# Kernel tuning notes

Hardware: AMD Instinct MI355X
Metric: run time of the kernel (lower is better)

## Reference

```python
import jax, jax.numpy as jnp
import numpy as np

D_MODEL = 1024
N_HEADS = 16
D_K = D_MODEL // N_HEADS  # 64
D_V = D_MODEL // N_HEADS  # 64
B, S = 2, 2048


def setup_inputs() -> dict:
    key = jax.random.key(0)
    ks = jax.random.split(key, 8)
    inp = {
        "Q": jax.random.normal(ks[0], (B, S, D_MODEL), dtype=jnp.float32),
        "K": jax.random.normal(ks[1], (B, S, D_MODEL), dtype=jnp.float32),
        "V": jax.random.normal(ks[2], (B, S, D_MODEL), dtype=jnp.float32),
        "prev": jax.random.normal(ks[3], (B, N_HEADS, S, S), dtype=jnp.float32) * 0.1,
        # torch nn.Linear weights are [out_features, in_features]
        "W_Q": jax.random.normal(ks[4], (N_HEADS * D_K, D_MODEL), dtype=jnp.float32) / np.sqrt(D_MODEL),
        "W_K": jax.random.normal(ks[5], (N_HEADS * D_K, D_MODEL), dtype=jnp.float32) / np.sqrt(D_MODEL),
        "W_V": jax.random.normal(ks[6], (N_HEADS * D_V, D_MODEL), dtype=jnp.float32) / np.sqrt(D_MODEL),
        "W_O": jax.random.normal(ks[7], (D_MODEL, N_HEADS * D_V), dtype=jnp.float32) / np.sqrt(N_HEADS * D_V),
    }
    return inp


def reference(Q, K, V, prev, W_Q, W_K, W_V, W_O):
    scale = D_K ** (-0.5)
    # projections: x @ W.T, then split heads -> (b, h, s, d)
    q = jnp.einsum('bsm,em->bse', Q, W_Q).reshape(B, S, N_HEADS, D_K).transpose(0, 2, 1, 3)
    k = jnp.einsum('bsm,em->bse', K, W_K).reshape(B, S, N_HEADS, D_K).transpose(0, 2, 1, 3)
    v = jnp.einsum('bsm,em->bse', V, W_V).reshape(B, S, N_HEADS, D_V).transpose(0, 2, 1, 3)
    scores = jnp.einsum('bhqd,bhkd->bhqk', q, k) * scale + prev
    attn = jax.nn.softmax(scores, axis=-1)  # attn_dropout = 0 (eval)
    context = jnp.einsum('bhqk,bhkd->bhqd', attn, v)
    context = context.transpose(0, 2, 1, 3).reshape(B, S, N_HEADS * D_V)
    output = jnp.einsum('bse,me->bsm', context, W_O)  # proj_dropout = 0 (eval)
    return (output, attn, scores)
```

## Files before the change

kernel.cpp:

```cpp
#include <hip/hip_runtime.h>

#define S_LEN 2048
#define NH 16
#define DH 64
#define DM 1024
#define NB 2
#define BS 4096

typedef __attribute__((ext_vector_type(4))) float f32x4;
typedef __attribute__((ext_vector_type(8))) short bfrag;

__device__ __forceinline__ unsigned short f2bf(float f) {
    unsigned u = __builtin_bit_cast(unsigned, f);
    u += 0x7FFFu + ((u >> 16) & 1u);
    return (unsigned short)(u >> 16);
}

__device__ __forceinline__ void gld16(const unsigned short* g, unsigned short* l) {
    __builtin_amdgcn_global_load_lds((const __attribute__((address_space(1))) void*)g,
                                     (__attribute__((address_space(3))) void*)l, 16, 0, 0);
}

__device__ __forceinline__ void lds_fence() {
    asm volatile("s_waitcnt lgkmcnt(0)" ::: "memory");
    __builtin_amdgcn_sched_barrier(0);
}

__global__ __launch_bounds__(256) void cast_all(const float* __restrict__ Q,
                                                const float* __restrict__ K,
                                                const float* __restrict__ V,
                                                const float* __restrict__ Wq,
                                                const float* __restrict__ Wk,
                                                const float* __restrict__ Wv,
                                                const float* __restrict__ Wo,
                                                unsigned short* __restrict__ Qc,
                                                unsigned short* __restrict__ Kc,
                                                unsigned short* __restrict__ Vc,
                                                unsigned short* __restrict__ Wqc,
                                                unsigned short* __restrict__ Wkc,
                                                unsigned short* __restrict__ Wvc,
                                                unsigned short* __restrict__ Woc) {
    int i = blockIdx.x * 256 + threadIdx.x;
    const float* src;
    unsigned short* dst;
    int off;
    if (i < 3145728) {
        int w = i >> 20;
        off = i & 1048575;
        src = (w == 0) ? Q : (w == 1) ? K : V;
        dst = (w == 0) ? Qc : (w == 1) ? Kc : Vc;
    } else {
        int j = i - 3145728;
        int w = j >> 18;
        off = j & 262143;
        src = (w == 0) ? Wq : (w == 1) ? Wk : (w == 2) ? Wv : Wo;
        dst = (w == 0) ? Wqc : (w == 1) ? Wkc : (w == 2) ? Wvc : Woc;
    }
    float4 v = reinterpret_cast<const float4*>(src)[off];
    ushort4 o;
    o.x = f2bf(v.x); o.y = f2bf(v.y); o.z = f2bf(v.z); o.w = f2bf(v.w);
    reinterpret_cast<ushort4*>(dst)[off] = o;
}

__global__ __launch_bounds__(256) void gemm_qkv(const unsigned short* __restrict__ Qc,
                                                const unsigned short* __restrict__ Kc,
                                                const unsigned short* __restrict__ Vc,
                                                const unsigned short* __restrict__ Wqc,
                                                const unsigned short* __restrict__ Wkc,
                                                const unsigned short* __restrict__ Wvc,
                                                unsigned short* __restrict__ qh,
                                                unsigned short* __restrict__ kh,
                                                unsigned short* __restrict__ vT) {
    const int z = blockIdx.z;
    const unsigned short* A = (z == 0) ? Qc : (z == 1) ? Kc : Vc;
    const unsigned short* B = (z == 0) ? Wqc : (z == 1) ? Wkc : Wvc;
    const int tid = threadIdx.x, lane = tid & 63;
    const int l15 = lane & 15, lhi = lane >> 4;
    const int w = tid >> 6, wr = w >> 1, wc = w & 1;
    const int m0 = blockIdx.y * 128, n0 = blockIdx.x * 128;
    const int K = DM;
    const int lr8 = lane >> 3;
    const int csw = (lane & 7) ^ lr8;

    __shared__ unsigned short sA[128 * 64];
    __shared__ unsigned short sB[128 * 64];

    f32x4 acc[4][4];
#pragma unroll
    for (int i = 0; i < 4; ++i)
#pragma unroll
        for (int j = 0; j < 4; ++j) acc[i][j] = (f32x4){0.f, 0.f, 0.f, 0.f};

    for (int t = 0; t < 16; ++t) {
        const int k0 = t * 64;
#pragma unroll
        for (int i = 0; i < 4; ++i) {
            int g = w * 4 + i;
            int row = g * 8 + lr8;
            gld16(A + (size_t)(m0 + row) * K + k0 + csw * 8, sA + g * 512);
            gld16(B + (size_t)(n0 + row) * K + k0 + csw * 8, sB + g * 512);
        }
        __syncthreads();
#pragma unroll
        for (int kk = 0; kk < 2; ++kk) {
            bfrag a[4], b[4];
#pragma unroll
            for (int f = 0; f < 4; ++f) {
                int ra = wr * 64 + f * 16 + l15;
                a[f] = *reinterpret_cast<const bfrag*>(
                    sA + ra * 64 + (((kk * 4 + lhi) ^ (ra & 7)) << 3));
                int rb = wc * 64 + f * 16 + l15;
                b[f] = *reinterpret_cast<const bfrag*>(
                    sB + rb * 64 + (((kk * 4 + lhi) ^ (rb & 7)) << 3));
            }
#pragma unroll
            for (int fm = 0; fm < 4; ++fm)
#pragma unroll
                for (int fn = 0; fn < 4; ++fn)
                    acc[fm][fn] =
                        __builtin_amdgcn_mfma_f32_16x16x32_bf16(a[fm], b[fn], acc[fm][fn], 0, 0, 0);
        }
        __syncthreads();
    }

    if (z == 2) {
#pragma unroll
        for (int fm = 0; fm < 4; ++fm)
#pragma unroll
            for (int fn = 0; fn < 4; ++fn) {
                int sbase = m0 + wr * 64 + fm * 16 + (lhi << 2);
                int gcol = n0 + wc * 64 + fn * 16 + l15;
                int b = sbase >> 11, s = sbase & 2047, h = gcol >> 6, d = gcol & 63;
                ushort4 o;
                o.x = f2bf(acc[fm][fn][0]); o.y = f2bf(acc[fm][fn][1]);
                o.z = f2bf(acc[fm][fn][2]); o.w = f2bf(acc[fm][fn][3]);
                *reinterpret_cast<ushort4*>(vT + ((size_t)(b * NH + h) * DH + d) * S_LEN + s) = o;
            }
    } else {
        unsigned short* Out = (z == 0) ? qh : kh;
#pragma unroll
        for (int fm = 0; fm < 4; ++fm)
#pragma unroll
            for (int fn = 0; fn < 4; ++fn)
#pragma unroll
                for (int r = 0; r < 4; ++r) {
                    int grow = m0 + wr * 64 + fm * 16 + (lhi << 2) + r;
                    int gcol = n0 + wc * 64 + fn * 16 + l15;
                    int b = grow >> 11, s = grow & 2047, h = gcol >> 6, d = gcol & 63;
                    Out[((size_t)(b * NH + h) * S_LEN + s) * DH + d] = f2bf(acc[fm][fn][r]);
                }
    }
}

__global__ __launch_bounds__(256) void gemm_out(const unsigned short* __restrict__ A,
                                                const unsigned short* __restrict__ B,
                                                float* __restrict__ Out) {
    const int tid = threadIdx.x, lane = tid & 63;
    const int l15 = lane & 15, lhi = lane >> 4;
    const int w = tid >> 6, wr = w >> 1, wc = w & 1;
    const int m0 = blockIdx.y * 128, n0 = blockIdx.x * 128;
    const int K = DM, N = DM;
    const int lr8 = lane >> 3;
    const int csw = (lane & 7) ^ lr8;

    __shared__ unsigned short sA[128 * 64];
    __shared__ unsigned short sB[128 * 64];

    f32x4 acc[4][4];
#pragma unroll
    for (int i = 0; i < 4; ++i)
#pragma unroll
        for (int j = 0; j < 4; ++j) acc[i][j] = (f32x4){0.f, 0.f, 0.f, 0.f};

    for (int t = 0; t < 16; ++t) {
        const int k0 = t * 64;
#pragma unroll
        for (int i = 0; i < 4; ++i) {
            int g = w * 4 + i;
            int row = g * 8 + lr8;
            gld16(A + (size_t)(m0 + row) * K + k0 + csw * 8, sA + g * 512);
            gld16(B + (size_t)(n0 + row) * K + k0 + csw * 8, sB + g * 512);
        }
        __syncthreads();
#pragma unroll
        for (int kk = 0; kk < 2; ++kk) {
            bfrag a[4], b[4];
#pragma unroll
            for (int f = 0; f < 4; ++f) {
                int ra = wr * 64 + f * 16 + l15;
                a[f] = *reinterpret_cast<const bfrag*>(
                    sA + ra * 64 + (((kk * 4 + lhi) ^ (ra & 7)) << 3));
                int rb = wc * 64 + f * 16 + l15;
                b[f] = *reinterpret_cast<const bfrag*>(
                    sB + rb * 64 + (((kk * 4 + lhi) ^ (rb & 7)) << 3));
            }
#pragma unroll
            for (int fm = 0; fm < 4; ++fm)
#pragma unroll
                for (int fn = 0; fn < 4; ++fn)
                    acc[fm][fn] =
                        __builtin_amdgcn_mfma_f32_16x16x32_bf16(a[fm], b[fn], acc[fm][fn], 0, 0, 0);
        }
        __syncthreads();
    }

#pragma unroll
    for (int fm = 0; fm < 4; ++fm)
#pragma unroll
        for (int fn = 0; fn < 4; ++fn)
#pragma unroll
            for (int r = 0; r < 4; ++r) {
                int grow = m0 + wr * 64 + fm * 16 + (lhi << 2) + r;
                int gcol = n0 + wc * 64 + fn * 16 + l15;
                Out[(size_t)grow * N + gcol] = acc[fm][fn][r];
            }
}

__global__ __launch_bounds__(64, 3) void attn_fused(const unsigned short* __restrict__ qh,
                                                    const unsigned short* __restrict__ kh,
                                                    const unsigned short* __restrict__ vT,
                                                    const float* __restrict__ prev,
                                                    float* __restrict__ scores,
                                                    float* __restrict__ attn,
                                                    unsigned short* __restrict__ ctx) {
    const int z = blockIdx.z;
    const int m0 = blockIdx.x * 16;
    const int lane = threadIdx.x & 63;
    const int l15 = lane & 15, lhi = lane >> 4;
    const int crow = lane >> 4;
    const int ccol = (lane & 15) * 4;

    __shared__ float sT[16 * 64];
    unsigned short* sB = reinterpret_cast<unsigned short*>(sT);

    const unsigned short* Qz = qh + (size_t)z * S_LEN * DH;
    const unsigned short* Kz = kh + (size_t)z * S_LEN * DH;
    const unsigned short* Vz = vT + (size_t)z * DH * S_LEN;
    const size_t zbase = (size_t)z * S_LEN * S_LEN;
    const float scale = 0.125f;

    size_t ro[4];
#pragma unroll
    for (int i = 0; i < 4; ++i)
        ro[i] = zbase + (size_t)(m0 + i * 4 + crow) * S_LEN + ccol;

    bfrag qf[2];
#pragma unroll
    for (int kk = 0; kk < 2; ++kk)
        qf[kk] = *reinterpret_cast<const bfrag*>(Qz + (size_t)(m0 + l15) * DH + kk * 32 +
                                                 lhi * 8);

    float m_r[4], l_r[4];
#pragma unroll
    for (int i = 0; i < 4; ++i) { m_r[i] = -1e30f; l_r[i] = 0.f; }

    bfrag kf[2][4];
#pragma unroll
    for (int kk = 0; kk < 2; ++kk)
#pragma unroll
        for (int f = 0; f < 4; ++f)
            kf[kk][f] = *reinterpret_cast<const bfrag*>(
                Kz + (size_t)(f * 16 + l15) * DH + kk * 32 + lhi * 8);
    f32x4 pv4[4];
#pragma unroll
    for (int i = 0; i < 4; ++i)
        pv4[i] = __builtin_nontemporal_load(reinterpret_cast<const f32x4*>(prev + ro[i]));

    for (int kt = 0; kt < 32; ++kt) {
        const int n0 = kt * 64;

        f32x4 acc[4];
#pragma unroll
        for (int f = 0; f < 4; ++f) acc[f] = (f32x4){0.f, 0.f, 0.f, 0.f};
#pragma unroll
        for (int kk = 0; kk < 2; ++kk)
#pragma unroll
            for (int f = 0; f < 4; ++f)
                acc[f] = __builtin_amdgcn_mfma_f32_16x16x32_bf16(kf[kk][f], qf[kk], acc[f], 0, 0, 0);

        if (kt < 31) {
            const int n1 = n0 + 64;
#pragma unroll
            for (int kk = 0; kk < 2; ++kk)
#pragma unroll
                for (int f = 0; f < 4; ++f)
                    kf[kk][f] = *reinterpret_cast<const bfrag*>(
                        Kz + (size_t)(n1 + f * 16 + l15) * DH + kk * 32 + lhi * 8);
        }

#pragma unroll
        for (int f = 0; f < 4; ++f)
            *reinterpret_cast<f32x4*>(sT + l15 * 64 + (((f * 4 + lhi) ^ (l15 & 7)) * 4)) = acc[f];
        lds_fence();
        f32x4 sc[4];
#pragma unroll
        for (int i = 0; i < 4; ++i) {
            int r = i * 4 + crow;
            sc[i] = *reinterpret_cast<const f32x4*>(sT + r * 64 + ((l15 ^ (r & 7)) * 4));
        }

#pragma unroll
        for (int i = 0; i < 4; ++i)
#pragma unroll
            for (int r = 0; r < 4; ++r) sc[i][r] = sc[i][r] * scale + pv4[i][r];
        if (kt < 31) {
            const int n1 = n0 + 64;
#pragma unroll
            for (int i = 0; i < 4; ++i)
                pv4[i] = __builtin_nontemporal_load(
                    reinterpret_cast<const f32x4*>(prev + ro[i] + n1));
        }
#pragma unroll
        for (int i = 0; i < 4; ++i)
            *reinterpret_cast<f32x4*>(scores + ro[i] + n0) = sc[i];

#pragma unroll
        for (int i = 0; i < 4; ++i) {
            float pm = fmaxf(fmaxf(sc[i][0], sc[i][1]), fmaxf(sc[i][2], sc[i][3]));
            pm = fmaxf(pm, __shfl_xor(pm, 1));
            pm = fmaxf(pm, __shfl_xor(pm, 2));
            pm = fmaxf(pm, __shfl_xor(pm, 4));
            pm = fmaxf(pm, __shfl_xor(pm, 8));
            float mnew = fmaxf(m_r[i], pm);
            float ps = __expf(sc[i][0] - mnew) + __expf(sc[i][1] - mnew) +
                       __expf(sc[i][2] - mnew) + __expf(sc[i][3] - mnew);
            ps += __shfl_xor(ps, 1);
            ps += __shfl_xor(ps, 2);
            ps += __shfl_xor(ps, 4);
            ps += __shfl_xor(ps, 8);
            l_r[i] = l_r[i] * __expf(m_r[i] - mnew) + ps;
            m_r[i] = mnew;
        }
    }

    float inv_l[4];
#pragma unroll
    for (int i = 0; i < 4; ++i) inv_l[i] = 1.0f / l_r[i];

    f32x4 acco[4];
#pragma unroll
    for (int f = 0; f < 4; ++f) acco[f] = (f32x4){0.f, 0.f, 0.f, 0.f};

    bfrag vf[2][4];
#pragma unroll
    for (int kk = 0; kk < 2; ++kk)
#pragma unroll
        for (int f = 0; f < 4; ++f)
            vf[kk][f] = *reinterpret_cast<const bfrag*>(
                Vz + (size_t)(f * 16 + l15) * S_LEN + 31 * 64 + kk * 32 + lhi * 8);
    f32x4 sv[4];
#pragma unroll
    for (int i = 0; i < 4; ++i)
        sv[i] = *reinterpret_cast<const f32x4*>(scores + ro[i] + 31 * 64);

    for (int kt = 31; kt >= 0; --kt) {
        const int n0 = kt * 64;
#pragma unroll
        for (int i = 0; i < 4; ++i) {
            int r = i * 4 + crow;
            f32x4 p4;
#pragma unroll
            for (int rr = 0; rr < 4; ++rr) p4[rr] = __expf(sv[i][rr] - m_r[i]) * inv_l[i];
            __builtin_nontemporal_store(p4, reinterpret_cast<f32x4*>(attn + ro[i] + n0));
            ushort4 pb;
            pb.x = f2bf(p4[0]); pb.y = f2bf(p4[1]); pb.z = f2bf(p4[2]); pb.w = f2bf(p4[3]);
            *reinterpret_cast<ushort4*>(sB + r * 64 + ((l15 ^ (r & 7)) * 4)) = pb;
        }
        lds_fence();
        bfrag pf[2];
#pragma unroll
        for (int kk = 0; kk < 2; ++kk) {
            int c0 = kk * 8 + lhi * 2;
            ushort4 lo = *reinterpret_cast<const ushort4*>(sB + l15 * 64 + ((c0 ^ (l15 & 7)) * 4));
            ushort4 hi =
                *reinterpret_cast<const ushort4*>(sB + l15 * 64 + (((c0 + 1) ^ (l15 & 7)) * 4));
            pf[kk][0] = (short)lo.x; pf[kk][1] = (short)lo.y;
            pf[kk][2] = (short)lo.z; pf[kk][3] = (short)lo.w;
            pf[kk][4] = (short)hi.x; pf[kk][5] = (short)hi.y;
            pf[kk][6] = (short)hi.z; pf[kk][7] = (short)hi.w;
        }
        if (kt > 0) {
            const int n1 = n0 - 64;
#pragma unroll
            for (int i = 0; i < 4; ++i)
                sv[i] = *reinterpret_cast<const f32x4*>(scores + ro[i] + n1);
        }
#pragma unroll
        for (int kk = 0; kk < 2; ++kk)
#pragma unroll
            for (int f = 0; f < 4; ++f)
                acco[f] = __builtin_amdgcn_mfma_f32_16x16x32_bf16(vf[kk][f], pf[kk], acco[f], 0, 0, 0);
        if (kt > 0) {
            const int n1 = n0 - 64;
#pragma unroll
            for (int kk = 0; kk < 2; ++kk)
#pragma unroll
                for (int f = 0; f < 4; ++f)
                    vf[kk][f] = *reinterpret_cast<const bfrag*>(
                        Vz + (size_t)(f * 16 + l15) * S_LEN + n1 + kk * 32 + lhi * 8);
        }
    }

    const int b = z >> 4, h = z & 15;
    const int s = m0 + l15;
#pragma unroll
    for (int f = 0; f < 4; ++f) {
        int d0 = f * 16 + lhi * 4;
        ushort4 o;
        o.x = f2bf(acco[f][0]); o.y = f2bf(acco[f][1]);
        o.z = f2bf(acco[f][2]); o.w = f2bf(acco[f][3]);
        *reinterpret_cast<ushort4*>(ctx + ((size_t)(b * S_LEN + s)) * DM + h * DH + d0) = o;
    }
}

extern "C" void kernel_launch(void* const* d_in, const int* in_sizes, int n_in, void* d_out,
                              int out_size, void* d_ws, size_t ws_size, hipStream_t stream) {
    const float* Q = (const float*)d_in[0];
    const float* K = (const float*)d_in[1];
    const float* V = (const float*)d_in[2];
    const float* prev = (const float*)d_in[3];
    const float* Wq = (const float*)d_in[4];
    const float* Wk = (const float*)d_in[5];
    const float* Wv = (const float*)d_in[6];
    const float* Wo = (const float*)d_in[7];

    float* out = (float*)d_out;
    float* attn = out + (size_t)BS * DM;
    float* scores = attn + (size_t)NB * NH * S_LEN * S_LEN;

    unsigned short* ws = (unsigned short*)d_ws;
    unsigned short* Qc = ws;
    unsigned short* Kc = Qc + (size_t)BS * DM;
    unsigned short* Vc = Kc + (size_t)BS * DM;
    unsigned short* Wqc = Vc + (size_t)BS * DM;
    unsigned short* Wkc = Wqc + (size_t)DM * DM;
    unsigned short* Wvc = Wkc + (size_t)DM * DM;
    unsigned short* Woc = Wvc + (size_t)DM * DM;
    unsigned short* qh = Woc + (size_t)DM * DM;
    unsigned short* kh = qh + (size_t)BS * DM;
    unsigned short* vT = kh + (size_t)BS * DM;
    unsigned short* ctx = vT + (size_t)BS * DM;

    cast_all<<<16384, 256, 0, stream>>>(Q, K, V, Wq, Wk, Wv, Wo,
                                        Qc, Kc, Vc, Wqc, Wkc, Wvc, Woc);

    dim3 gq(DM / 128, BS / 128, 3);
    gemm_qkv<<<gq, 256, 0, stream>>>(Qc, Kc, Vc, Wqc, Wkc, Wvc, qh, kh, vT);

    dim3 ga(S_LEN / 16, 1, NB * NH);
    attn_fused<<<ga, 64, 0, stream>>>(qh, kh, vT, prev, scores, attn, ctx);

    dim3 gp(DM / 128, BS / 128, 1);
    gemm_out<<<gp, 256, 0, stream>>>(ctx, Woc, out);
}
```

Measured before the change: 631.4 us.

## Split fused attention into scores/stats and softmax-PV kernels with 4-wave blocks

Splits the single-wave fused attention kernel into two kernels. The first computes scores and stores the per-row max and sum to a workspace buffer; the second recomputes the probabilities, writes attn and does the PV matmul. Blocks grow to 4 waves, and the second kernel is launched in reverse block order, likely so it reads recently written scores while they may still be in cache. Software prefetching of the K, V, prev and scores tiles is dropped in favour of plain in-loop loads. This adds a kernel launch and a small stats round trip.

Result: slower. 646.8 us (+2.4%).

```diff
diff --git a/kernel.cpp b/kernel.cpp
--- a/kernel.cpp
+++ b/kernel.cpp
@@ -216,26 +216,25 @@
             }
 }
 
-__global__ __launch_bounds__(64, 3) void attn_fused(const unsigned short* __restrict__ qh,
-                                                    const unsigned short* __restrict__ kh,
-                                                    const unsigned short* __restrict__ vT,
-                                                    const float* __restrict__ prev,
-                                                    float* __restrict__ scores,
-                                                    float* __restrict__ attn,
-                                                    unsigned short* __restrict__ ctx) {
+__global__ __launch_bounds__(256, 4) void scores_stats(const unsigned short* __restrict__ qh,
+                                                       const unsigned short* __restrict__ kh,
+                                                       const float* __restrict__ prev,
+                                                       float* __restrict__ scores,
+                                                       float* __restrict__ m_buf,
+                                                       float* __restrict__ l_buf) {
     const int z = blockIdx.z;
-    const int m0 = blockIdx.x * 16;
+    const int w = threadIdx.x >> 6;
+    const int m0 = blockIdx.x * 64 + w * 16;
     const int lane = threadIdx.x & 63;
     const int l15 = lane & 15, lhi = lane >> 4;
     const int crow = lane >> 4;
     const int ccol = (lane & 15) * 4;
 
-    __shared__ float sT[16 * 64];
-    unsigned short* sB = reinterpret_cast<unsigned short*>(sT);
+    __shared__ float sTall[4][16 * 64];
+    float* sT = sTall[w];
 
     const unsigned short* Qz = qh + (size_t)z * S_LEN * DH;
     const unsigned short* Kz = kh + (size_t)z * S_LEN * DH;
-    const unsigned short* Vz = vT + (size_t)z * DH * S_LEN;
     const size_t zbase = (size_t)z * S_LEN * S_LEN;
     const float scale = 0.125f;
 
@@ -254,20 +253,20 @@
 #pragma unroll
     for (int i = 0; i < 4; ++i) { m_r[i] = -1e30f; l_r[i] = 0.f; }
 
-    bfrag kf[2][4];
-#pragma unroll
-    for (int kk = 0; kk < 2; ++kk)
-#pragma unroll
-        for (int f = 0; f < 4; ++f)
-            kf[kk][f] = *reinterpret_cast<const bfrag*>(
-                Kz + (size_t)(f * 16 + l15) * DH + kk * 32 + lhi * 8);
-    f32x4 pv4[4];
-#pragma unroll
-    for (int i = 0; i < 4; ++i)
-        pv4[i] = __builtin_nontemporal_load(reinterpret_cast<const f32x4*>(prev + ro[i]));
-
     for (int kt = 0; kt < 32; ++kt) {
         const int n0 = kt * 64;
+        bfrag kf[2][4];
+#pragma unroll
+        for (int kk = 0; kk < 2; ++kk)
+#pragma unroll
+            for (int f = 0; f < 4; ++f)
+                kf[kk][f] = *reinterpret_cast<const bfrag*>(
+                    Kz + (size_t)(n0 + f * 16 + l15) * DH + kk * 32 + lhi * 8);
+        f32x4 pv4[4];
+#pragma unroll
+        for (int i = 0; i < 4; ++i)
+            pv4[i] = __builtin_nontemporal_load(
+                reinterpret_cast<const f32x4*>(prev + ro[i] + n0));
 
         f32x4 acc[4];
 #pragma unroll
@@ -277,16 +276,6 @@
 #pragma unroll
             for (int f = 0; f < 4; ++f)
                 acc[f] = __builtin_amdgcn_mfma_f32_16x16x32_bf16(kf[kk][f], qf[kk], acc[f], 0, 0, 0);
-
-        if (kt < 31) {
-            const int n1 = n0 + 64;
-#pragma unroll
-            for (int kk = 0; kk < 2; ++kk)
-#pragma unroll
-                for (int f = 0; f < 4; ++f)
-                    kf[kk][f] = *reinterpret_cast<const bfrag*>(
-                        Kz + (size_t)(n1 + f * 16 + l15) * DH + kk * 32 + lhi * 8);
-        }
 
 #pragma unroll
         for (int f = 0; f < 4; ++f)
@@ -298,18 +287,10 @@
             int r = i * 4 + crow;
             sc[i] = *reinterpret_cast<const f32x4*>(sT + r * 64 + ((l15 ^ (r & 7)) * 4));
         }
-
 #pragma unroll
         for (int i = 0; i < 4; ++i)
 #pragma unroll
             for (int r = 0; r < 4; ++r) sc[i][r] = sc[i][r] * scale + pv4[i][r];
-        if (kt < 31) {
-            const int n1 = n0 + 64;
-#pragma unroll
-            for (int i = 0; i < 4; ++i)
-                pv4[i] = __builtin_nontemporal_load(
-                    reinterpret_cast<const f32x4*>(prev + ro[i] + n1));
-        }
 #pragma unroll
         for (int i = 0; i < 4; ++i)
             *reinterpret_cast<f32x4*>(scores + ro[i] + n0) = sc[i];
@@ -333,28 +314,67 @@
         }
     }
 
-    float inv_l[4];
-#pragma unroll
-    for (int i = 0; i < 4; ++i) inv_l[i] = 1.0f / l_r[i];
+    if (l15 == 0) {
+#pragma unroll
+        for (int i = 0; i < 4; ++i) {
+            size_t row = (size_t)z * S_LEN + m0 + i * 4 + crow;
+            m_buf[row] = m_r[i];
+            l_buf[row] = l_r[i];
+        }
+    }
+}
+
+__global__ __launch_bounds__(256, 4) void softmax_pv(const float* __restrict__ scores,
+                                                     const unsigned short* __restrict__ vT,
+                                                     const float* __restrict__ m_buf,
+                                                     const float* __restrict__ l_buf,
+                                                     float* __restrict__ attn,
+                                                     unsigned short* __restrict__ ctx) {
+    const int z = (NB * NH - 1) - blockIdx.z;
+    const int w = threadIdx.x >> 6;
+    const int m0 = (31 - blockIdx.x) * 64 + w * 16;
+    const int lane = threadIdx.x & 63;
+    const int l15 = lane & 15, lhi = lane >> 4;
+    const int crow = lane >> 4;
+    const int ccol = (lane & 15) * 4;
+
+    __shared__ unsigned short sBall[4][16 * 64];
+    unsigned short* sB = sBall[w];
+
+    const unsigned short* Vz = vT + (size_t)z * DH * S_LEN;
+    const size_t zbase = (size_t)z * S_LEN * S_LEN;
+
+    size_t ro[4];
+#pragma unroll
+    for (int i = 0; i < 4; ++i)
+        ro[i] = zbase + (size_t)(m0 + i * 4 + crow) * S_LEN + ccol;
+
+    float m_r[4], inv_l[4];
+#pragma unroll
+    for (int i = 0; i < 4; ++i) {
+        size_t row = (size_t)z * S_LEN + m0 + i * 4 + crow;
+        m_r[i] = m_buf[row];
+        inv_l[i] = 1.0f / l_buf[row];
+    }
 
     f32x4 acco[4];
 #pragma unroll
     for (int f = 0; f < 4; ++f) acco[f] = (f32x4){0.f, 0.f, 0.f, 0.f};
-
-    bfrag vf[2][4];
-#pragma unroll
-    for (int kk = 0; kk < 2; ++kk)
-#pragma unroll
-        for (int f = 0; f < 4; ++f)
-            vf[kk][f] = *reinterpret_cast<const bfrag*>(
-                Vz + (size_t)(f * 16 + l15) * S_LEN + 31 * 64 + kk * 32 + lhi * 8);
-    f32x4 sv[4];
-#pragma unroll
-    for (int i = 0; i < 4; ++i)
-        sv[i] = *reinterpret_cast<const f32x4*>(scores + ro[i] + 31 * 64);
 
     for (int kt = 31; kt >= 0; --kt) {
         const int n0 = kt * 64;
+        bfrag vf[2][4];
+#pragma unroll
+        for (int kk = 0; kk < 2; ++kk)
+#pragma unroll
+            for (int f = 0; f < 4; ++f)
+                vf[kk][f] = *reinterpret_cast<const bfrag*>(
+                    Vz + (size_t)(f * 16 + l15) * S_LEN + n0 + kk * 32 + lhi * 8);
+        f32x4 sv[4];
+#pragma unroll
+        for (int i = 0; i < 4; ++i)
+            sv[i] = *reinterpret_cast<const f32x4*>(scores + ro[i] + n0);
+
 #pragma unroll
         for (int i = 0; i < 4; ++i) {
             int r = i * 4 + crow;
@@ -371,7 +391,8 @@
 #pragma unroll
         for (int kk = 0; kk < 2; ++kk) {
             int c0 = kk * 8 + lhi * 2;
-            ushort4 lo = *reinterpret_cast<const ushort4*>(sB + l15 * 64 + ((c0 ^ (l15 & 7)) * 4));
+            ushort4 lo =
+                *reinterpret_cast<const ushort4*>(sB + l15 * 64 + ((c0 ^ (l15 & 7)) * 4));
             ushort4 hi =
                 *reinterpret_cast<const ushort4*>(sB + l15 * 64 + (((c0 + 1) ^ (l15 & 7)) * 4));
             pf[kk][0] = (short)lo.x; pf[kk][1] = (short)lo.y;
@@ -379,26 +400,12 @@
             pf[kk][4] = (short)hi.x; pf[kk][5] = (short)hi.y;
             pf[kk][6] = (short)hi.z; pf[kk][7] = (short)hi.w;
         }
-        if (kt > 0) {
-            const int n1 = n0 - 64;
-#pragma unroll
-            for (int i = 0; i < 4; ++i)
-                sv[i] = *reinterpret_cast<const f32x4*>(scores + ro[i] + n1);
-        }
 #pragma unroll
         for (int kk = 0; kk < 2; ++kk)
 #pragma unroll
             for (int f = 0; f < 4; ++f)
-                acco[f] = __builtin_amdgcn_mfma_f32_16x16x32_bf16(vf[kk][f], pf[kk], acco[f], 0, 0, 0);
-        if (kt > 0) {
-            const int n1 = n0 - 64;
-#pragma unroll
-            for (int kk = 0; kk < 2; ++kk)
-#pragma unroll
-                for (int f = 0; f < 4; ++f)
-                    vf[kk][f] = *reinterpret_cast<const bfrag*>(
-                        Vz + (size_t)(f * 16 + l15) * S_LEN + n1 + kk * 32 + lhi * 8);
-        }
+                acco[f] =
+                    __builtin_amdgcn_mfma_f32_16x16x32_bf16(vf[kk][f], pf[kk], acco[f], 0, 0, 0);
     }
 
     const int b = z >> 4, h = z & 15;
@@ -440,6 +447,8 @@
     unsigned short* kh = qh + (size_t)BS * DM;
     unsigned short* vT = kh + (size_t)BS * DM;
     unsigned short* ctx = vT + (size_t)BS * DM;
+    float* m_buf = (float*)(ctx + (size_t)BS * DM);
+    float* l_buf = m_buf + (size_t)NB * NH * S_LEN;
 
     cast_all<<<16384, 256, 0, stream>>>(Q, K, V, Wq, Wk, Wv, Wo,
                                         Qc, Kc, Vc, Wqc, Wkc, Wvc, Woc);
@@ -447,8 +456,10 @@
     dim3 gq(DM / 128, BS / 128, 3);
     gemm_qkv<<<gq, 256, 0, stream>>>(Qc, Kc, Vc, Wqc, Wkc, Wvc, qh, kh, vT);
 
-    dim3 ga(S_LEN / 16, 1, NB * NH);
-    attn_fused<<<ga, 64, 0, stream>>>(qh, kh, vT, prev, scores, attn, ctx);
+    dim3 g1(S_LEN / 64, 1, NB * NH);
+    scores_stats<<<g1, 256, 0, stream>>>(qh, kh, prev, scores, m_buf, l_buf);
+
+    softmax_pv<<<g1, 256, 0, stream>>>(scores, vT, m_buf, l_buf, attn, ctx);
 
     dim3 gp(DM / 128, BS / 128, 1);
     gemm_out<<<gp, 256, 0, stream>>>(ctx, Woc, out);
```
